# Kernel tuning notes

Measured on AMD Instinct MI355X. Metric: run time of the kernel, lower is better.

Reference implementation:

```python
import jax, jax.numpy as jnp
import numpy as np

EMBED = 1024
KEY = 64
HEAD = 64
CTX = 4096
BATCH = 8


def _linear(x, w, b):
    # torch nn.Linear: y = x @ W.T + b, W shape [out, in]
    return x @ w.T + b


def setup_inputs() -> dict:
    key = jax.random.key(0)
    ks = jax.random.split(key, 11)
    s_e = 1.0 / np.sqrt(EMBED)
    s_k = 1.0 / np.sqrt(KEY)
    return {
        "embeddings": jax.random.normal(ks[0], (BATCH, CTX, EMBED), dtype=jnp.float32),
        "kw1": jax.random.uniform(ks[1], (KEY, EMBED), jnp.float32, -s_e, s_e),
        "kb1": jax.random.uniform(ks[2], (KEY,), jnp.float32, -s_e, s_e),
        "kw2": jax.random.uniform(ks[3], (KEY, KEY), jnp.float32, -s_k, s_k),
        "kb2": jax.random.uniform(ks[4], (KEY,), jnp.float32, -s_k, s_k),
        "qw1": jax.random.uniform(ks[5], (KEY, EMBED), jnp.float32, -s_e, s_e),
        "qb1": jax.random.uniform(ks[6], (KEY,), jnp.float32, -s_e, s_e),
        "qw2": jax.random.uniform(ks[7], (KEY, KEY), jnp.float32, -s_k, s_k),
        "qb2": jax.random.uniform(ks[8], (KEY,), jnp.float32, -s_k, s_k),
        "vw": jax.random.uniform(ks[9], (HEAD, EMBED), jnp.float32, -s_e, s_e),
        "vb": jax.random.uniform(ks[10], (HEAD,), jnp.float32, -s_e, s_e),
    }


def reference(embeddings, kw1, kb1, kw2, kb2, qw1, qb1, qw2, qb2, vw, vb):
    T = embeddings.shape[1]
    keys = jax.nn.relu(_linear(jax.nn.relu(_linear(embeddings, kw1, kb1)), kw2, kb2))
    queries = jax.nn.relu(_linear(jax.nn.relu(_linear(embeddings, qw1, qb1)), qw2, qb2))
    values = _linear(embeddings, vw, vb)
    # scores: [B, T, T]
    scores = jnp.einsum("btk,bsk->bts", queries, keys) / np.sqrt(KEY).astype(np.float32)
    # Faithful to original: tril(ones) * -1e10 added (masks lower triangle incl. diagonal)
    mask = jnp.tril(jnp.ones((T, T), dtype=jnp.float32)) * jnp.float32(-1e10)
    weights = jax.nn.softmax(scores + mask, axis=-1)
    return jnp.einsum("bts,bsh->bth", weights, values)
```

## Files before the change

kernel.cpp:

```cpp
#include <hip/hip_runtime.h>
#include <hip/hip_bf16.h>
#include <math.h>

#define NB   8
#define TCTX 4096
#define ED   1024
#define KD   64

typedef __attribute__((ext_vector_type(8))) short bf16x8;
typedef __attribute__((ext_vector_type(4))) float f32x4;

#define LOG2E  1.44269504088896340736f
#define SCALE2 (0.125f * LOG2E)
#define MASK2  (-1e10f * LOG2E)

__device__ __forceinline__ void lds_fence() {
    asm volatile("s_waitcnt lgkmcnt(0)" ::: "memory");
    __builtin_amdgcn_sched_barrier(0);
}

__device__ __forceinline__ unsigned short f2bf(float f) {
    union { float f; unsigned u; } c; c.f = f;
    return (unsigned short)((c.u + 0x7FFFu + ((c.u >> 16) & 1u)) >> 16);
}
__device__ __forceinline__ int swz(int row, int byteoff) {
    return row * 128 + (byteoff ^ ((row & 7) << 4));
}
__device__ __forceinline__ f32x4 fzero4() {
    f32x4 z; z[0] = 0.f; z[1] = 0.f; z[2] = 0.f; z[3] = 0.f; return z;
}
__device__ __forceinline__ void gl_lds16(const void* g, void* l) {
    __builtin_amdgcn_global_load_lds(
        (const __attribute__((address_space(1))) unsigned int*)g,
        (__attribute__((address_space(3))) unsigned int*)l, 16, 0, 0);
}
__device__ __forceinline__ unsigned cvtpk_bf16(float lo, float hi) {
    unsigned r;
    asm("v_cvt_pk_bf16_f32 %0, %1, %2" : "=v"(r) : "v"(lo), "v"(hi));
    return r;
}

__global__ __launch_bounds__(256) void prep_kernel(
    const float* __restrict__ kw1, const float* __restrict__ qw1,
    const float* __restrict__ vw,  const float* __restrict__ kw2,
    const float* __restrict__ qw2,
    unsigned short* __restrict__ W1p, unsigned short* __restrict__ W2p)
{
    int idx = blockIdx.x * 256 + threadIdx.x;
    if (idx < 24576) {
        int ks = idx / 1536, rem = idx % 1536;
        int r = rem >> 3, bb = rem & 7;
        int c = bb ^ (r & 7);
        const float* src = (r < 64)  ? (kw1 + r * ED)
                         : (r < 128) ? (qw1 + (r - 64) * ED)
                                     : (vw  + (r - 128) * ED);
        src += ks * 64 + c * 8;
        unsigned short* dst = W1p + (size_t)idx * 8;
        #pragma unroll
        for (int e = 0; e < 8; ++e) dst[e] = f2bf(src[e]);
    } else if (idx < 25600) {
        int j = idx - 24576;
        int lane = j & 63, kh = (j >> 6) & 1, n = (j >> 7) & 3, kq = j >> 9;
        int row = n * 16 + (lane & 15);
        int ko  = kh * 32 + (lane >> 4) * 8;
        const float* src = (kq ? qw2 : kw2) + row * 64 + ko;
        unsigned short* dst = W2p + (size_t)j * 8;
        #pragma unroll
        for (int e = 0; e < 8; ++e) dst[e] = f2bf(src[e]);
    }
}

__global__ __launch_bounds__(256, 2) void proj_kernel(
    const float* __restrict__ emb,
    const unsigned short* __restrict__ W1p, const unsigned short* __restrict__ W2p,
    const float* __restrict__ kb1, const float* __restrict__ kb2,
    const float* __restrict__ qb1, const float* __restrict__ qb2,
    const float* __restrict__ vb,
    unsigned short* __restrict__ Qo, unsigned short* __restrict__ Ko,
    unsigned short* __restrict__ Vt)
{
    __shared__ __align__(16) char lds[80 * 1024];

    const int tid  = threadIdx.x;
    const int lane = tid & 63;
    const int w    = tid >> 6;
    const int lr   = lane & 15;
    const int lg   = lane >> 4;
    const long r0  = (long)blockIdx.x * 64;
    const int  b   = blockIdx.x >> 6;
    const int  tb  = (blockIdx.x & 63) * 64;

    const float* embB = emb + r0 * ED;

    f32x4 acc[12];
    #pragma unroll
    for (int j = 0; j < 12; ++j) acc[j] = fzero4();

    auto stageA = [&](int buf, int ks) {
        char* Abuf = lds + buf * 16 * 1024;
        const float* eb = embB + ks * 64;
        #pragma unroll
        for (int j = 0; j < 4; ++j) {
            int chunk = j * 4 + w;
            int r = chunk * 4 + (lane >> 4);
            int c = (lane & 15) ^ (r & 7);
            gl_lds16(eb + (long)r * ED + c * 4, Abuf + chunk * 1024);
        }
    };
    auto stageB = [&](int buf, int ks) {
        char* Bbuf = lds + 32 * 1024 + buf * 24 * 1024;
        const unsigned short* wb = W1p + (size_t)ks * 12288;
        #pragma unroll
        for (int j = 0; j < 6; ++j) {
            int chunk = j * 4 + w;
            gl_lds16(wb + chunk * 512 + lane * 8, Bbuf + chunk * 1024);
        }
    };

    stageA(0, 0); stageB(0, 0);
    __syncthreads();

    int cur = 0;
    for (int ks = 0; ks < 16; ++ks) {
        if (ks < 15) { stageA(cur ^ 1, ks + 1); stageB(cur ^ 1, ks + 1); }
        char* Ac = lds + cur * 16 * 1024;
        char* Bc = lds + 32 * 1024 + cur * 24 * 1024;
        const int r = w * 16 + lr;
        #pragma unroll
        for (int kh = 0; kh < 2; ++kh) {
            int cb0 = kh * 8 + lg * 2;
            float4 fa = *(const float4*)(Ac + r * 256 + ((cb0 ^ (r & 7)) * 16));
            float4 fb = *(const float4*)(Ac + r * 256 + (((cb0 + 1) ^ (r & 7)) * 16));
            bf16x8 a;
            a[0] = (short)f2bf(fa.x); a[1] = (short)f2bf(fa.y);
            a[2] = (short)f2bf(fa.z); a[3] = (short)f2bf(fa.w);
            a[4] = (short)f2bf(fb.x); a[5] = (short)f2bf(fb.y);
            a[6] = (short)f2bf(fb.z); a[7] = (short)f2bf(fb.w);
            #pragma unroll
            for (int n = 0; n < 12; ++n) {
                bf16x8 bv = *(const bf16x8*)(Bc + swz(n * 16 + lr, kh * 64 + lg * 16));
                acc[n] = __builtin_amdgcn_mfma_f32_16x16x32_bf16(a, bv, acc[n], 0, 0, 0);
            }
        }
        __syncthreads();
        cur ^= 1;
    }

    char* H  = lds + w * 2048;
    char* VT = lds + 16 * 1024;

    #pragma unroll
    for (int kq = 0; kq < 2; ++kq) {
        const float* b1 = kq ? qb1 : kb1;
        const float* b2 = kq ? qb2 : kb2;
        unsigned short* dst = kq ? Qo : Ko;
        const float oscale = kq ? SCALE2 : 1.0f;
        #pragma unroll
        for (int n = 0; n < 4; ++n) {
            int col = n * 16 + lr;
            float bias = b1[col];
            #pragma unroll
            for (int rr = 0; rr < 4; ++rr) {
                int row = lg * 4 + rr;
                *(unsigned short*)(H + swz(row, col * 2)) =
                    f2bf(fmaxf(acc[kq * 4 + n][rr] + bias, 0.f));
            }
        }
        lds_fence();
        bf16x8 a2k0 = *(const bf16x8*)(H + swz(lr, 0 * 64 + lg * 16));
        bf16x8 a2k1 = *(const bf16x8*)(H + swz(lr, 1 * 64 + lg * 16));
        lds_fence();

        f32x4 acc2[4];
        #pragma unroll
        for (int n = 0; n < 4; ++n) acc2[n] = fzero4();
        #pragma unroll
        for (int n = 0; n < 4; ++n) {
            bf16x8 w2f0 = *(const bf16x8*)(W2p + ((kq * 4 + n) * 2 + 0) * 512 + lane * 8);
            bf16x8 w2f1 = *(const bf16x8*)(W2p + ((kq * 4 + n) * 2 + 1) * 512 + lane * 8);
            acc2[n] = __builtin_amdgcn_mfma_f32_16x16x32_bf16(a2k0, w2f0, acc2[n], 0, 0, 0);
            acc2[n] = __builtin_amdgcn_mfma_f32_16x16x32_bf16(a2k1, w2f1, acc2[n], 0, 0, 0);
        }
        #pragma unroll
        for (int n = 0; n < 4; ++n) {
            int col = n * 16 + lr;
            float bias = b2[col];
            #pragma unroll
            for (int rr = 0; rr < 4; ++rr) {
                long rg = r0 + w * 16 + lg * 4 + rr;
                dst[rg * KD + col] = f2bf(fmaxf(acc2[n][rr] + bias, 0.f) * oscale);
            }
        }
    }

    #pragma unroll
    for (int n = 0; n < 4; ++n) {
        int col = n * 16 + lr;
        float bias = vb[col];
        #pragma unroll
        for (int rr = 0; rr < 4; ++rr) {
            int tl = w * 16 + lg * 4 + rr;
            *(unsigned short*)(VT + swz(col, tl * 2)) = f2bf(acc[8 + n][rr] + bias);
        }
    }
    __syncthreads();
    #pragma unroll
    for (int it = 0; it < 2; ++it) {
        int c = it * 256 + tid;
        int h = c >> 3, c4 = c & 7;
        *(int4*)(Vt + ((long)b * KD + h) * TCTX + tb + c4 * 8) =
            *(const int4*)(VT + swz(h, c4 * 16));
    }
}

__global__ __launch_bounds__(128) void attn_kernel(
    const unsigned short* __restrict__ Qb,
    const unsigned short* __restrict__ Kb,
    const unsigned short* __restrict__ Vt,
    float* __restrict__ Opart, float2* __restrict__ MSum)
{
    __shared__ __align__(16) char lds[20 * 1024];

    const int bid  = blockIdx.x;
    const int half = bid & 1;
    const int rest = bid >> 1;
    const int b    = rest & 7;
    const int qr   = rest >> 3;
    const int qi   = (qr + 127) & 127;
    const int t0   = qi * 32;
    const int tid = threadIdx.x, lane = tid & 63, w = tid >> 6;
    const int lr  = lane & 15, lg = lane >> 4;
    const int tg  = t0 + w * 16 + lr;

    char* Kl = lds;
    char* Vl = lds + 8 * 1024;
    char* QP = lds + 16 * 1024 + w * 2048;

    const unsigned short* Qg  = Qb + ((long)b * TCTX + t0 + w * 16) * KD;
    const unsigned short* Kg0 = Kb + (long)b * TCTX * KD;
    const unsigned short* Vg0 = Vt + (long)b * KD * TCTX;

    const int srow = lane >> 3;
    const int sblk = lane & 7;

    const int s0q = (qi == 127) ? 0 : (qi >> 1);
    const int len = 64 - s0q;
    const int mid = s0q + ((len + 1) >> 1);
    const int s_lo = half ? mid : s0q;
    const int s_hi = half ? 64  : mid;

    auto stageK = [&](int si) {
        const unsigned short* Kg = Kg0 + si * 64 * KD;
        #pragma unroll
        for (int j = 0; j < 4; ++j) {
            int chunk = w * 4 + j;
            int r = chunk * 8 + srow;
            int c = sblk ^ (r & 7);
            gl_lds16(Kg + r * KD + c * 8, Kl + chunk * 1024);
        }
    };
    auto stageV = [&](int si) {
        const unsigned short* Vg = Vg0 + si * 64;
        #pragma unroll
        for (int j = 0; j < 4; ++j) {
            int chunk = w * 4 + j;
            int r = chunk * 8 + srow;
            int c = sblk ^ (r & 7);
            gl_lds16(Vg + (long)r * TCTX + c * 8, Vl + chunk * 1024);
        }
    };

    float m2 = MASK2, sum_p = 0.f;
    f32x4 O[4];
    #pragma unroll
    for (int n = 0; n < 4; ++n) O[n] = fzero4();

    if (s_lo < s_hi) {
        #pragma unroll
        for (int j = 0; j < 2; ++j) {
            int r = j * 8 + srow;
            int c = sblk ^ (r & 7);
            gl_lds16(Qg + r * KD + c * 8, QP + j * 1024);
        }
        stageK(s_lo);
        stageV(s_lo);
        __syncthreads();

        bf16x8 qf[2];
        #pragma unroll
        for (int kh = 0; kh < 2; ++kh)
            qf[kh] = *(const bf16x8*)(QP + swz(lr, kh * 64 + lg * 16));

        for (int si = s_lo; si < s_hi; ++si) {
            f32x4 sc[4];
            #pragma unroll
            for (int mi = 0; mi < 4; ++mi) sc[mi] = fzero4();
            __builtin_amdgcn_s_setprio(1);
            #pragma unroll
            for (int kh = 0; kh < 2; ++kh) {
                #pragma unroll
                for (int mi = 0; mi < 4; ++mi) {
                    bf16x8 kf = *(const bf16x8*)(Kl + swz(mi * 16 + lr, kh * 64 + lg * 16));
                    sc[mi] = __builtin_amdgcn_mfma_f32_16x16x32_bf16(kf, qf[kh], sc[mi], 0, 0, 0);
                }
            }
            __builtin_amdgcn_s_setprio(0);

            __syncthreads();
            if (si + 1 < s_hi) stageK(si + 1);

            const int thr = tg - si * 64;
            float s2v[4][4];
            #pragma unroll
            for (int mi = 0; mi < 4; ++mi)
                #pragma unroll
                for (int rr = 0; rr < 4; ++rr) {
                    int sl = mi * 16 + lg * 4 + rr;
                    s2v[mi][rr] = (sl <= thr) ? MASK2 : sc[mi][rr];
                }

            float pml = s2v[0][0];
            #pragma unroll
            for (int mi = 0; mi < 4; ++mi)
                #pragma unroll
                for (int rr = 0; rr < 4; ++rr) pml = fmaxf(pml, s2v[mi][rr]);

            if (!__all(pml - m2 <= 8.0f)) {
                float pm = pml;
                pm = fmaxf(pm, __shfl_xor(pm, 16, 64));
                pm = fmaxf(pm, __shfl_xor(pm, 32, 64));
                float mnew = fmaxf(m2, pm);
                float scl = __builtin_amdgcn_exp2f(m2 - mnew);
                m2 = mnew;
                sum_p *= scl;
                #pragma unroll
                for (int rr = 0; rr < 4; ++rr) {
                    float sb = __shfl(scl, lg * 4 + rr, 64);
                    #pragma unroll
                    for (int n = 0; n < 4; ++n) O[n][rr] *= sb;
                }
            }
            float ls = 0.f;
            #pragma unroll
            for (int mi = 0; mi < 4; ++mi)
                #pragma unroll
                for (int rr = 0; rr < 4; ++rr) {
                    s2v[mi][rr] = __builtin_amdgcn_exp2f(s2v[mi][rr] - m2);
                    ls += s2v[mi][rr];
                }
            sum_p += ls;

            #pragma unroll
            for (int mi = 0; mi < 4; ++mi) {
                unsigned lo = cvtpk_bf16(s2v[mi][0], s2v[mi][1]);
                unsigned hi = cvtpk_bf16(s2v[mi][2], s2v[mi][3]);
                *(uint2*)(QP + swz(lr, mi * 32 + lg * 8)) = make_uint2(lo, hi);
            }
            lds_fence();
            bf16x8 ap0 = *(const bf16x8*)(QP + swz(lr, 0 * 64 + lg * 16));
            bf16x8 ap1 = *(const bf16x8*)(QP + swz(lr, 1 * 64 + lg * 16));
            lds_fence();

            __builtin_amdgcn_s_setprio(1);
            #pragma unroll
            for (int n = 0; n < 4; ++n) {
                bf16x8 bv0 = *(const bf16x8*)(Vl + swz(n * 16 + lr, 0 * 64 + lg * 16));
                bf16x8 bv1 = *(const bf16x8*)(Vl + swz(n * 16 + lr, 1 * 64 + lg * 16));
                O[n] = __builtin_amdgcn_mfma_f32_16x16x32_bf16(ap0, bv0, O[n], 0, 0, 0);
                O[n] = __builtin_amdgcn_mfma_f32_16x16x32_bf16(ap1, bv1, O[n], 0, 0, 0);
            }
            __builtin_amdgcn_s_setprio(0);

            __syncthreads();
            if (si + 1 < s_hi) stageV(si + 1);
        }
    }

    float sr = sum_p;
    sr += __shfl_xor(sr, 16, 64);
    sr += __shfl_xor(sr, 32, 64);
    const long rbase = (long)b * TCTX + t0 + w * 16;
    #pragma unroll
    for (int rr = 0; rr < 4; ++rr) {
        int tl = lg * 4 + rr;
        long rowi = (rbase + tl) * 2 + half;
        #pragma unroll
        for (int n = 0; n < 4; ++n)
            Opart[rowi * 64 + n * 16 + lr] = O[n][rr];
    }
    if (lg == 0)
        MSum[(rbase + lr) * 2 + half] = make_float2(m2, sr);
}

__global__ __launch_bounds__(256) void combine_kernel(
    const float* __restrict__ Opart, const float2* __restrict__ MSum,
    float* __restrict__ out)
{
    const long total = (long)NB * TCTX * KD;
    for (long idx = (long)blockIdx.x * 256 + threadIdx.x; idx < total;
         idx += (long)gridDim.x * 256) {
        long r = idx >> 6;
        int  h = (int)(idx & 63);
        float2 A = MSum[r * 2 + 0];
        float2 B = MSum[r * 2 + 1];
        float M  = fmaxf(A.x, B.x);
        float wa = __builtin_amdgcn_exp2f(A.x - M);
        float wb = __builtin_amdgcn_exp2f(B.x - M);
        float denom = A.y * wa + B.y * wb;
        float oa = Opart[(r * 2 + 0) * 64 + h];
        float ob = Opart[(r * 2 + 1) * 64 + h];
        out[idx] = (oa * wa + ob * wb) / denom;
    }
}

extern "C" void kernel_launch(void* const* d_in, const int* in_sizes, int n_in,
                              void* d_out, int out_size, void* d_ws, size_t ws_size,
                              hipStream_t stream) {
    const float* emb = (const float*)d_in[0];
    const float* kw1 = (const float*)d_in[1];
    const float* kb1 = (const float*)d_in[2];
    const float* kw2 = (const float*)d_in[3];
    const float* kb2 = (const float*)d_in[4];
    const float* qw1 = (const float*)d_in[5];
    const float* qb1 = (const float*)d_in[6];
    const float* qw2 = (const float*)d_in[7];
    const float* qb2 = (const float*)d_in[8];
    const float* vw  = (const float*)d_in[9];
    const float* vb  = (const float*)d_in[10];

    unsigned short* Qb  = (unsigned short*)d_ws;
    unsigned short* Kb  = Qb + (size_t)NB * TCTX * KD;
    unsigned short* Vt  = Kb + (size_t)NB * TCTX * KD;
    unsigned short* W1p = Vt + (size_t)NB * TCTX * KD;
    unsigned short* W2p = W1p + 196608;
    float*  Opart = (float*)(W2p + 8192);
    float2* MSum  = (float2*)(Opart + (size_t)NB * TCTX * 2 * KD);

    hipLaunchKernelGGL(prep_kernel, dim3(100), dim3(256), 0, stream,
                       kw1, qw1, vw, kw2, qw2, W1p, W2p);
    hipLaunchKernelGGL(proj_kernel, dim3(512), dim3(256), 0, stream,
                       emb, W1p, W2p, kb1, kb2, qb1, qb2, vb,
                       Qb, Kb, Vt);
    hipLaunchKernelGGL(attn_kernel, dim3(2048), dim3(128), 0, stream,
                       Qb, Kb, Vt, Opart, MSum);
    hipLaunchKernelGGL(combine_kernel, dim3(2048), dim3(256), 0, stream,
                       Opart, MSum, (float*)d_out);
}
```

Before: 85.40 us.

## Double-buffer K tiles in LDS and load V fragments directly into registers

The K tile now uses two LDS buffers, so the next tile is prefetched at the top of each iteration and one barrier per iteration is dropped. V is no longer staged through LDS. Each lane loads its V fragments straight from global memory into registers, where they feed the PV MFMAs. The kernel also adds a min-blocks-per-CU hint of 4 in the launch bounds. The trade is more register pressure and uncoalesced strided global reads of V in exchange for fewer barriers and better overlap of loads with compute.

```diff
diff --git a/kernel.cpp b/kernel.cpp
--- a/kernel.cpp
+++ b/kernel.cpp
@@ -213,7 +213,7 @@
     }
 }
 
-__global__ __launch_bounds__(128) void attn_kernel(
+__global__ __launch_bounds__(128, 4) void attn_kernel(
     const unsigned short* __restrict__ Qb,
     const unsigned short* __restrict__ Kb,
     const unsigned short* __restrict__ Vt,
@@ -232,8 +232,6 @@
     const int lr  = lane & 15, lg = lane >> 4;
     const int tg  = t0 + w * 16 + lr;
 
-    char* Kl = lds;
-    char* Vl = lds + 8 * 1024;
     char* QP = lds + 16 * 1024 + w * 2048;
 
     const unsigned short* Qg  = Qb + ((long)b * TCTX + t0 + w * 16) * KD;
@@ -249,7 +247,8 @@
     const int s_lo = half ? mid : s0q;
     const int s_hi = half ? 64  : mid;
 
-    auto stageK = [&](int si) {
+    auto stageK = [&](int buf, int si) {
+        char* Kl = lds + buf * 8 * 1024;
         const unsigned short* Kg = Kg0 + si * 64 * KD;
         #pragma unroll
         for (int j = 0; j < 4; ++j) {
@@ -259,16 +258,6 @@
             gl_lds16(Kg + r * KD + c * 8, Kl + chunk * 1024);
         }
     };
-    auto stageV = [&](int si) {
-        const unsigned short* Vg = Vg0 + si * 64;
-        #pragma unroll
-        for (int j = 0; j < 4; ++j) {
-            int chunk = w * 4 + j;
-            int r = chunk * 8 + srow;
-            int c = sblk ^ (r & 7);
-            gl_lds16(Vg + (long)r * TCTX + c * 8, Vl + chunk * 1024);
-        }
-    };
 
     float m2 = MASK2, sum_p = 0.f;
     f32x4 O[4];
@@ -282,8 +271,7 @@
             int c = sblk ^ (r & 7);
             gl_lds16(Qg + r * KD + c * 8, QP + j * 1024);
         }
-        stageK(s_lo);
-        stageV(s_lo);
+        stageK(0, s_lo);
         __syncthreads();
 
         bf16x8 qf[2];
@@ -291,7 +279,20 @@
         for (int kh = 0; kh < 2; ++kh)
             qf[kh] = *(const bf16x8*)(QP + swz(lr, kh * 64 + lg * 16));
 
+        int cur = 0;
         for (int si = s_lo; si < s_hi; ++si) {
+            if (si + 1 < s_hi) stageK(cur ^ 1, si + 1);
+
+            const unsigned short* Vg = Vg0 + si * 64;
+            bf16x8 vf[2][4];
+            #pragma unroll
+            for (int kh = 0; kh < 2; ++kh)
+                #pragma unroll
+                for (int n = 0; n < 4; ++n)
+                    vf[kh][n] = *(const bf16x8*)(Vg + (long)(n * 16 + lr) * TCTX + kh * 32 + lg * 8);
+
+            char* Kl = lds + cur * 8 * 1024;
+
             f32x4 sc[4];
             #pragma unroll
             for (int mi = 0; mi < 4; ++mi) sc[mi] = fzero4();
@@ -305,9 +306,6 @@
                 }
             }
             __builtin_amdgcn_s_setprio(0);
-
-            __syncthreads();
-            if (si + 1 < s_hi) stageK(si + 1);
 
             const int thr = tg - si * 64;
             float s2v[4][4];
@@ -364,15 +362,13 @@
             __builtin_amdgcn_s_setprio(1);
             #pragma unroll
             for (int n = 0; n < 4; ++n) {
-                bf16x8 bv0 = *(const bf16x8*)(Vl + swz(n * 16 + lr, 0 * 64 + lg * 16));
-                bf16x8 bv1 = *(const bf16x8*)(Vl + swz(n * 16 + lr, 1 * 64 + lg * 16));
-                O[n] = __builtin_amdgcn_mfma_f32_16x16x32_bf16(ap0, bv0, O[n], 0, 0, 0);
-                O[n] = __builtin_amdgcn_mfma_f32_16x16x32_bf16(ap1, bv1, O[n], 0, 0, 0);
+                O[n] = __builtin_amdgcn_mfma_f32_16x16x32_bf16(ap0, vf[0][n], O[n], 0, 0, 0);
+                O[n] = __builtin_amdgcn_mfma_f32_16x16x32_bf16(ap1, vf[1][n], O[n], 0, 0, 0);
             }
             __builtin_amdgcn_s_setprio(0);
 
             __syncthreads();
-            if (si + 1 < s_hi) stageV(si + 1);
+            cur ^= 1;
         }
     }
 
```

Result: slower. 124.5 us (+45.8%).

## Double-buffer V tiles and redistribute P via shuffles instead of LDS

Applied to the files above, without the earlier changes.

Adds a second V buffer in LDS so the next V tile is prefetched along with the next K tile right after the score MFMAs, giving it more time to land before use. The P tile is no longer round-tripped through LDS: the bf16-packed probabilities are moved into MFMA A-operand layout with cross-lane shuffles, removing two LDS fences. The block index mapping also changes so batch varies fastest across consecutive blocks. The cost is 4KB more LDS per block, which may reduce occupancy, and 16 shuffles per iteration.

```diff
diff --git a/kernel.cpp b/kernel.cpp
--- a/kernel.cpp
+++ b/kernel.cpp
@@ -219,23 +219,18 @@
     const unsigned short* __restrict__ Vt,
     float* __restrict__ Opart, float2* __restrict__ MSum)
 {
-    __shared__ __align__(16) char lds[20 * 1024];
+    __shared__ __align__(16) char lds[24 * 1024];
 
     const int bid  = blockIdx.x;
-    const int half = bid & 1;
-    const int rest = bid >> 1;
-    const int b    = rest & 7;
-    const int qr   = rest >> 3;
+    const int b    = bid & 7;
+    const int half = (bid >> 3) & 1;
+    const int qr   = bid >> 4;
     const int qi   = (qr + 127) & 127;
     const int t0   = qi * 32;
     const int tid = threadIdx.x, lane = tid & 63, w = tid >> 6;
     const int lr  = lane & 15, lg = lane >> 4;
     const int tg  = t0 + w * 16 + lr;
 
-    char* Kl = lds;
-    char* Vl = lds + 8 * 1024;
-    char* QP = lds + 16 * 1024 + w * 2048;
-
     const unsigned short* Qg  = Qb + ((long)b * TCTX + t0 + w * 16) * KD;
     const unsigned short* Kg0 = Kb + (long)b * TCTX * KD;
     const unsigned short* Vg0 = Vt + (long)b * KD * TCTX;
@@ -256,10 +251,11 @@
             int chunk = w * 4 + j;
             int r = chunk * 8 + srow;
             int c = sblk ^ (r & 7);
-            gl_lds16(Kg + r * KD + c * 8, Kl + chunk * 1024);
+            gl_lds16(Kg + r * KD + c * 8, lds + chunk * 1024);
         }
     };
-    auto stageV = [&](int si) {
+    auto stageV = [&](int buf, int si) {
+        char* Vl = lds + 8 * 1024 + buf * 8 * 1024;
         const unsigned short* Vg = Vg0 + si * 64;
         #pragma unroll
         for (int j = 0; j < 4; ++j) {
@@ -276,6 +272,7 @@
     for (int n = 0; n < 4; ++n) O[n] = fzero4();
 
     if (s_lo < s_hi) {
+        char* QP = lds + 16 * 1024 + w * 2048;
         #pragma unroll
         for (int j = 0; j < 2; ++j) {
             int r = j * 8 + srow;
@@ -283,7 +280,7 @@
             gl_lds16(Qg + r * KD + c * 8, QP + j * 1024);
         }
         stageK(s_lo);
-        stageV(s_lo);
+        stageV(0, s_lo);
         __syncthreads();
 
         bf16x8 qf[2];
@@ -291,6 +288,7 @@
         for (int kh = 0; kh < 2; ++kh)
             qf[kh] = *(const bf16x8*)(QP + swz(lr, kh * 64 + lg * 16));
 
+        int cur = 0;
         for (int si = s_lo; si < s_hi; ++si) {
             f32x4 sc[4];
             #pragma unroll
@@ -300,14 +298,17 @@
             for (int kh = 0; kh < 2; ++kh) {
                 #pragma unroll
                 for (int mi = 0; mi < 4; ++mi) {
-                    bf16x8 kf = *(const bf16x8*)(Kl + swz(mi * 16 + lr, kh * 64 + lg * 16));
+                    bf16x8 kf = *(const bf16x8*)(lds + swz(mi * 16 + lr, kh * 64 + lg * 16));
                     sc[mi] = __builtin_amdgcn_mfma_f32_16x16x32_bf16(kf, qf[kh], sc[mi], 0, 0, 0);
                 }
             }
             __builtin_amdgcn_s_setprio(0);
 
             __syncthreads();
-            if (si + 1 < s_hi) stageK(si + 1);
+            if (si + 1 < s_hi) {
+                stageK(si + 1);
+                stageV(cur ^ 1, si + 1);
+            }
 
             const int thr = tg - si * 64;
             float s2v[4][4];
@@ -350,29 +351,39 @@
                 }
             sum_p += ls;
 
+            unsigned W[4][2];
             #pragma unroll
             for (int mi = 0; mi < 4; ++mi) {
-                unsigned lo = cvtpk_bf16(s2v[mi][0], s2v[mi][1]);
-                unsigned hi = cvtpk_bf16(s2v[mi][2], s2v[mi][3]);
-                *(uint2*)(QP + swz(lr, mi * 32 + lg * 8)) = make_uint2(lo, hi);
-            }
-            lds_fence();
-            bf16x8 ap0 = *(const bf16x8*)(QP + swz(lr, 0 * 64 + lg * 16));
-            bf16x8 ap1 = *(const bf16x8*)(QP + swz(lr, 1 * 64 + lg * 16));
-            lds_fence();
-
+                W[mi][0] = cvtpk_bf16(s2v[mi][0], s2v[mi][1]);
+                W[mi][1] = cvtpk_bf16(s2v[mi][2], s2v[mi][3]);
+            }
+            const int lgh  = lg >> 1;
+            const int bsrc = 2 * (lg & 1);
+            union { unsigned u[4]; bf16x8 v; } apu0, apu1;
+            #pragma unroll
+            for (int jj = 0; jj < 4; ++jj) {
+                int srcl = ((bsrc + (jj >> 1)) << 4) | lr;
+                unsigned lo0 = __shfl(W[0][jj & 1], srcl, 64);
+                unsigned hi0 = __shfl(W[1][jj & 1], srcl, 64);
+                unsigned lo1 = __shfl(W[2][jj & 1], srcl, 64);
+                unsigned hi1 = __shfl(W[3][jj & 1], srcl, 64);
+                apu0.u[jj] = lgh ? hi0 : lo0;
+                apu1.u[jj] = lgh ? hi1 : lo1;
+            }
+
+            char* Vl = lds + 8 * 1024 + cur * 8 * 1024;
             __builtin_amdgcn_s_setprio(1);
             #pragma unroll
             for (int n = 0; n < 4; ++n) {
                 bf16x8 bv0 = *(const bf16x8*)(Vl + swz(n * 16 + lr, 0 * 64 + lg * 16));
                 bf16x8 bv1 = *(const bf16x8*)(Vl + swz(n * 16 + lr, 1 * 64 + lg * 16));
-                O[n] = __builtin_amdgcn_mfma_f32_16x16x32_bf16(ap0, bv0, O[n], 0, 0, 0);
-                O[n] = __builtin_amdgcn_mfma_f32_16x16x32_bf16(ap1, bv1, O[n], 0, 0, 0);
+                O[n] = __builtin_amdgcn_mfma_f32_16x16x32_bf16(apu0.v, bv0, O[n], 0, 0, 0);
+                O[n] = __builtin_amdgcn_mfma_f32_16x16x32_bf16(apu1.v, bv1, O[n], 0, 0, 0);
             }
             __builtin_amdgcn_s_setprio(0);
 
             __syncthreads();
-            if (si + 1 < s_hi) stageV(si + 1);
+            cur ^= 1;
         }
     }
 
```

New measurement: 91.46 us. +7.1%, slower.
